# Kernel tuning notes

Measured on AMD Instinct MI355X. Metric: run time of the kernel, lower is better.

The kernel has to match this reference:

```python
import jax, jax.numpy as jnp
import numpy as np

B, C, H, W = 16, 256, 128, 128
NF = 8
GN_GROUPS = 8
EPS = 1e-5


def setup_inputs() -> dict:
    key = jax.random.key(0)
    k0, k1, k2, k3 = jax.random.split(key, 4)
    return {
        "x": jax.random.normal(k0, (B, C, H, W), dtype=jnp.float32),
        # learned params
        "filter_bank": jax.random.normal(k1, (NF, 1, 7, 7), dtype=jnp.float32) * 0.02,
        "sel_w": jax.random.normal(k2, (NF, C), dtype=jnp.float32) / np.float32(np.sqrt(C)),
        "sel_b": jnp.zeros((NF,), dtype=jnp.float32),
        "proj_w": jax.random.normal(k3, (C, C, 1, 1), dtype=jnp.float32) / np.float32(np.sqrt(C)),
        "proj_b": jnp.zeros((C,), dtype=jnp.float32),
        "gn_gamma": jnp.ones((C,), dtype=jnp.float32),
        "gn_beta": jnp.zeros((C,), dtype=jnp.float32),
    }


def reference(x, filter_bank, sel_w, sel_b, proj_w, proj_b, gn_gamma, gn_beta):
    b, c, h, w = x.shape
    # filter selector: GAP -> Linear -> softmax
    pooled = x.mean(axis=(2, 3))                       # [B, C]
    weights = jax.nn.softmax(pooled @ sel_w.T + sel_b, axis=-1)  # [B, NF]
    # softmax-weighted mix of the 7x7 filter bank -> one filter per sample
    combined = jnp.einsum('bn,nhw->bhw', weights, filter_bank[:, 0])  # [B, 7, 7]
    # per-sample depthwise conv: each sample's filter applied to all C channels
    kern = jnp.repeat(combined[:, None], c, axis=0)    # [B*C, 1, 7, 7] (sample-major, matches reshape)
    filtered = jax.lax.conv_general_dilated(
        x.reshape(1, b * c, h, w), kern,
        window_strides=(1, 1), padding=((3, 3), (3, 3)),
        feature_group_count=b * c,
        dimension_numbers=('NCHW', 'OIHW', 'NCHW'),
    ).reshape(b, c, h, w)
    # output projection: 1x1 conv
    y = jnp.einsum('bchw,oc->bohw', filtered, proj_w[:, :, 0, 0]) + proj_b[None, :, None, None]
    # GroupNorm(8, C) with affine
    yg = y.reshape(b, GN_GROUPS, c // GN_GROUPS, h, w)
    mean = yg.mean(axis=(2, 3, 4), keepdims=True)
    var = yg.var(axis=(2, 3, 4), keepdims=True)
    yn = ((yg - mean) * jax.lax.rsqrt(var + EPS)).reshape(b, c, h, w)
    yn = yn * gn_gamma[None, :, None, None] + gn_beta[None, :, None, None]
    # exact GELU (torch default) + residual
    return jax.nn.gelu(yn, approximate=False) + x
```

## Files before the change

kernel.cpp:

```cpp
#include <hip/hip_runtime.h>
#include <math.h>

#define BB 16
#define CC 256
#define HH 128
#define WW 128
#define HWSZ 16384
#define NF 8
#define EPSV 1e-5f

typedef __attribute__((ext_vector_type(8))) short short8;
typedef __attribute__((ext_vector_type(4))) float f32x4;

static __device__ __forceinline__ unsigned short f2bf(float f) {
  unsigned int u = __float_as_uint(f);
  u += 0x7fffu + ((u >> 16) & 1u);
  return (unsigned short)(u >> 16);
}

static __device__ __forceinline__ float bf2f(unsigned int h) {
  return __uint_as_float(h << 16);
}

static __device__ __forceinline__ void gload_lds16(const unsigned short* g,
                                                   unsigned short* l) {
  __builtin_amdgcn_global_load_lds(
      (const __attribute__((address_space(1))) void*)(size_t)g,
      (__attribute__((address_space(3))) void*)(unsigned)(size_t)l, 16, 0, 0);
}

__global__ __launch_bounds__(256) void pack_a_kernel(
    const float* __restrict__ pw, unsigned short* __restrict__ ap) {
  int idx = blockIdx.x * 256 + threadIdx.x;
  int e = idx & 7;
  int lane = (idx >> 3) & 63;
  int kb = (idx >> 9) & 7;
  int mb = idx >> 12;
  int o = mb * 16 + (lane & 15);
  int c = kb * 32 + (lane >> 4) * 8 + e;
  ap[idx] = f2bf(pw[o * 256 + c]);
}

__global__ __launch_bounds__(256) void pool_kernel(
    const float* __restrict__ x, float* __restrict__ pooled) {
  int plane = blockIdx.x;
  const float4* xp = (const float4*)(x + (size_t)plane * HWSZ);
  int tid = threadIdx.x;
  float s = 0.f;
#pragma unroll
  for (int i = 0; i < 16; ++i) {
    float4 v = xp[tid + i * 256];
    s += v.x + v.y + v.z + v.w;
  }
#pragma unroll
  for (int off = 32; off > 0; off >>= 1) s += __shfl_down(s, off, 64);
  __shared__ float ls[4];
  if ((tid & 63) == 0) ls[tid >> 6] = s;
  __syncthreads();
  if (tid == 0) pooled[plane] = (ls[0] + ls[1] + ls[2] + ls[3]) * (1.0f / 16384.0f);
}

__global__ __launch_bounds__(256) void selector_kernel(
    const float* __restrict__ pooled, const float* __restrict__ sel_w,
    const float* __restrict__ sel_b, const float* __restrict__ fbank,
    float* __restrict__ combined) {
  int tid = threadIdx.x;
  __shared__ float lg[BB][NF];
  __shared__ float wsm[BB][NF];
  if (tid < BB * NF) {
    int b = tid >> 3, n = tid & 7;
    const float* p = pooled + b * CC;
    const float* w = sel_w + n * CC;
    float d = sel_b[n];
    for (int c = 0; c < CC; c += 4) {
      d += p[c] * w[c] + p[c + 1] * w[c + 1] + p[c + 2] * w[c + 2] + p[c + 3] * w[c + 3];
    }
    lg[b][n] = d;
  }
  __syncthreads();
  if (tid < BB) {
    int b = tid;
    float m = lg[b][0];
#pragma unroll
    for (int n = 1; n < NF; ++n) m = fmaxf(m, lg[b][n]);
    float e[NF];
    float s = 0.f;
#pragma unroll
    for (int n = 0; n < NF; ++n) { e[n] = expf(lg[b][n] - m); s += e[n]; }
    float inv = 1.0f / s;
#pragma unroll
    for (int n = 0; n < NF; ++n) wsm[b][n] = e[n] * inv;
  }
  __syncthreads();
  for (int i = tid; i < BB * 49; i += 256) {
    int b = i / 49, j = i % 49;
    float acc = 0.f;
#pragma unroll
    for (int n = 0; n < NF; ++n) acc += wsm[b][n] * fbank[n * 49 + j];
    combined[b * 64 + j] = acc;
  }
}

#define TR 32
__global__ __launch_bounds__(256) void dwconv_kernel(
    const float* __restrict__ x, const float* __restrict__ combined,
    unsigned short* __restrict__ fbp) {
  int plane = blockIdx.x;
  int rt = blockIdx.y;
  int b = plane >> 8;
  int r0 = rt * TR;
  int tid = threadIdx.x;

  __shared__ float xs[TR + 6][136];

  float kf[49];
  {
    const float* cb = combined + b * 64;
#pragma unroll
    for (int i = 0; i < 49; ++i) kf[i] = cb[i];
  }

  const size_t pbase = (size_t)plane * HWSZ;
  for (int idx = tid; idx < (TR + 6) * 34; idx += 256) {
    int row = idx / 34;
    int seg = idx % 34;
    int r = r0 - 3 + row;
    int c = seg * 4 - 4;
    float4 v = make_float4(0.f, 0.f, 0.f, 0.f);
    if (r >= 0 && r < HH && c >= 0 && c < WW) {
      v = *(const float4*)(x + pbase + (size_t)r * WW + c);
    }
    *(float4*)&xs[row][seg * 4] = v;
  }
  __syncthreads();

  int cg = tid & 31;
  int rg = tid >> 5;
  float acc[4][4] = {};

#pragma unroll
  for (int ri = 0; ri < 10; ++ri) {
    int lrow = 4 * rg + ri;
    float xr[12];
#pragma unroll
    for (int s = 0; s < 3; ++s)
      *(float4*)&xr[4 * s] = *(const float4*)&xs[lrow][cg * 4 + 4 * s];
#pragma unroll
    for (int orr = 0; orr < 4; ++orr) {
      int dy = ri - orr;
      if (dy < 0 || dy > 6) continue;
#pragma unroll
      for (int oc = 0; oc < 4; ++oc) {
#pragma unroll
        for (int dx = 0; dx < 7; ++dx) {
          acc[orr][oc] += xr[oc + dx + 1] * kf[dy * 7 + dx];
        }
      }
    }
  }

#pragma unroll
  for (int orr = 0; orr < 4; ++orr) {
    ushort4 sv;
    sv.x = f2bf(acc[orr][0]);
    sv.y = f2bf(acc[orr][1]);
    sv.z = f2bf(acc[orr][2]);
    sv.w = f2bf(acc[orr][3]);
    *(ushort4*)(fbp + pbase + (size_t)(r0 + 4 * rg + orr) * WW + 4 * cg) = sv;
  }
}

__global__ __launch_bounds__(256) void transpose_kernel(
    const unsigned short* __restrict__ fb, unsigned short* __restrict__ fbT) {
  int bid = blockIdx.x;
  int bs = bid >> 10;
  int cs = (bid >> 8) & 3;
  int ps = bid & 255;
  int t = threadIdx.x;

  __shared__ unsigned int Ts[64][33];

  int cpair = t >> 3;
  int pch = t & 7;
  const unsigned short* s =
      fb + ((size_t)bs * CC + cs * 64 + 2 * cpair) * HWSZ + ps * 64 + pch * 8;
  uint4 A0 = *(const uint4*)s;
  uint4 A1 = *(const uint4*)(s + HWSZ);
  unsigned int wa[4] = {A0.x, A0.y, A0.z, A0.w};
  unsigned int wb[4] = {A1.x, A1.y, A1.z, A1.w};
#pragma unroll
  for (int i = 0; i < 8; ++i) {
    int p = pch * 8 + i;
    unsigned int lo = (wa[i >> 1] >> ((i & 1) * 16)) & 0xffffu;
    unsigned int hi = (wb[i >> 1] >> ((i & 1) * 16)) & 0xffffu;
    Ts[p][cpair] = lo | (hi << 16);
  }
  __syncthreads();

  size_t obase = ((size_t)bs * HWSZ + (size_t)ps * 64) * 256 + cs * 64;
#pragma unroll
  for (int r = 0; r < 2; ++r) {
    int chunk = t + 256 * r;
    int p = chunk >> 3, ch = chunk & 7;
    uint4 v;
    v.x = Ts[p][ch * 4];
    v.y = Ts[p][ch * 4 + 1];
    v.z = Ts[p][ch * 4 + 2];
    v.w = Ts[p][ch * 4 + 3];
    *(uint4*)(fbT + obase + (size_t)p * 256 + ch * 8) = v;
  }
}

#define SWZ(p) ((((p) >> 1) ^ ((p) >> 4)) & 3)

__global__ __launch_bounds__(512, 4) void gemm_kernel(
    const unsigned short* __restrict__ fbT, const unsigned short* __restrict__ ap,
    const float* __restrict__ proj_b, unsigned short* __restrict__ yb,
    float* __restrict__ part) {
  int bid = blockIdx.x;
  int bs = bid >> 8;
  int ot = (bid >> 7) & 1;
  int pt = bid & 127;
  int p0 = pt * 128;
  int tid = threadIdx.x;
  int lane = tid & 63;
  int wave = tid >> 6;
  int wm = wave >> 2;
  int wn = wave & 3;

  __shared__ __align__(16) unsigned short A_lds[2][4096];
  __shared__ __align__(16) unsigned short B_lds[2][4096];

  const unsigned short* asrc0 =
      ap + (((size_t)(ot * 8 + (tid >> 6)) * 8) * 64 + (tid & 63)) * 8;
  unsigned short* adst = &A_lds[0][0] + (size_t)tid * 8;
  int sp = tid >> 2;
  int sj = (tid & 3) ^ SWZ(sp);
  const unsigned short* bsrc0 =
      fbT + ((size_t)bs * HWSZ + p0 + sp) * 256 + sj * 8;
  unsigned short* bdst = &B_lds[0][0] + (size_t)tid * 8;

#define STAGE(kb, buf)                                                  \
  do {                                                                  \
    gload_lds16(asrc0 + (size_t)(kb) * 512, adst + (size_t)(buf) * 4096); \
    gload_lds16(bsrc0 + (size_t)(kb) * 32, bdst + (size_t)(buf) * 4096);  \
  } while (0)

  STAGE(0, 0);
  STAGE(1, 1);

  f32x4 acc[4][2];
#pragma unroll
  for (int mb = 0; mb < 4; ++mb)
#pragma unroll
    for (int nb = 0; nb < 2; ++nb) acc[mb][nb] = (f32x4){0.f, 0.f, 0.f, 0.f};

  int aofs[4];
#pragma unroll
  for (int mb = 0; mb < 4; ++mb) aofs[mb] = ((wm * 4 + mb) * 64 + lane) * 8;
  int bofs[2];
#pragma unroll
  for (int nb = 0; nb < 2; ++nb) {
    int pp = wn * 32 + nb * 16 + (lane & 15);
    bofs[nb] = pp * 32 + (((lane >> 4) * 8) ^ (SWZ(pp) << 3));
  }

#pragma unroll
  for (int kb = 0; kb < 8; ++kb) {
    const int cur = kb & 1;
    if (kb < 7) {
      asm volatile("s_waitcnt vmcnt(2)" ::: "memory");
    } else {
      asm volatile("s_waitcnt vmcnt(0)" ::: "memory");
    }
    __builtin_amdgcn_s_barrier();

    short8 af[4], bfr[2];
#pragma unroll
    for (int mb = 0; mb < 4; ++mb)
      af[mb] = *(const short8*)(&A_lds[cur][0] + aofs[mb]);
#pragma unroll
    for (int nb = 0; nb < 2; ++nb)
      bfr[nb] = *(const short8*)(&B_lds[cur][0] + bofs[nb]);
    asm volatile("s_waitcnt lgkmcnt(0)" ::: "memory");
    __builtin_amdgcn_sched_barrier(0);
    __builtin_amdgcn_s_barrier();

    if (kb < 6) STAGE(kb + 2, cur);
    __builtin_amdgcn_sched_barrier(0);

#pragma unroll
    for (int mb = 0; mb < 4; ++mb)
#pragma unroll
      for (int nb = 0; nb < 2; ++nb)
        acc[mb][nb] = __builtin_amdgcn_mfma_f32_16x16x32_bf16(
            af[mb], bfr[nb], acc[mb][nb], 0, 0, 0);
  }

  float psum[2] = {0.f, 0.f}, psq[2] = {0.f, 0.f};
  int orl = (lane >> 4) * 4;
  int pl = lane & 15;
  const size_t ybase = (size_t)bs * CC * HWSZ + p0 + wn * 32;
  int obase = ot * 128 + wm * 64;
#pragma unroll
  for (int mb = 0; mb < 4; ++mb) {
    int gi = mb >> 1;
#pragma unroll
    for (int r = 0; r < 4; ++r) {
      int o = obase + mb * 16 + orl + r;
      float pb = proj_b[o];
      unsigned short* yrow = yb + ybase + (size_t)o * HWSZ + pl;
#pragma unroll
      for (int nb = 0; nb < 2; ++nb) {
        float v = acc[mb][nb][r] + pb;
        yrow[nb * 16] = f2bf(v);
        psum[gi] += v;
        psq[gi] += v * v;
      }
    }
  }
#pragma unroll
  for (int off = 32; off > 0; off >>= 1) {
#pragma unroll
    for (int k = 0; k < 2; ++k) {
      psum[k] += __shfl_down(psum[k], off, 64);
      psq[k] += __shfl_down(psq[k], off, 64);
    }
  }
  if (lane == 0) {
#pragma unroll
    for (int k = 0; k < 2; ++k) {
      int bg = bs * 8 + ot * 4 + wm * 2 + k;
      part[(size_t)bg * 512 + pt * 4 + wn] = psum[k];
      part[65536 + (size_t)bg * 512 + pt * 4 + wn] = psq[k];
    }
  }
#undef STAGE
}

__global__ __launch_bounds__(256) void reduce_kernel(
    const float* __restrict__ part, float* __restrict__ stats) {
  int bg = blockIdx.x;
  int t = threadIdx.x;
  const float* ps = part + (size_t)bg * 512;
  const float* pq = part + 65536 + (size_t)bg * 512;
  float s = ps[t] + ps[t + 256];
  float q = pq[t] + pq[t + 256];
#pragma unroll
  for (int off = 32; off > 0; off >>= 1) {
    s += __shfl_down(s, off, 64);
    q += __shfl_down(q, off, 64);
  }
  __shared__ float ls[8];
  if ((t & 63) == 0) { ls[t >> 6] = s; ls[4 + (t >> 6)] = q; }
  __syncthreads();
  if (t == 0) stats[bg] = ls[0] + ls[1] + ls[2] + ls[3];
  if (t == 64) stats[128 + bg] = ls[4] + ls[5] + ls[6] + ls[7];
}

__global__ __launch_bounds__(256) void out_kernel(
    const float* __restrict__ x, const unsigned short* __restrict__ yb,
    const float* __restrict__ stats, const float* __restrict__ gamma,
    const float* __restrict__ beta, float* __restrict__ out) {
  int plane = blockIdx.x;
  int b = plane >> 8, c = plane & 255, g = c >> 5;
  const float inv_n = 1.0f / (32.0f * (float)HWSZ);
  float mean = stats[b * 8 + g] * inv_n;
  float var = stats[128 + b * 8 + g] * inv_n - mean * mean;
  float rstd = rsqrtf(var + EPSV);
  float scale = gamma[c] * rstd;
  float shift = beta[c] - mean * scale;

  const size_t base = (size_t)plane * HWSZ;
  for (int i = threadIdx.x; i < HWSZ / 8; i += 256) {
    uint4 yv = *(const uint4*)(yb + base + 8 * (size_t)i);
    float4 x0 = *(const float4*)(x + base + 8 * (size_t)i);
    float4 x1 = *(const float4*)(x + base + 8 * (size_t)i + 4);
    unsigned int yw[4] = {yv.x, yv.y, yv.z, yv.w};
    float r[8];
    float xr[8] = {x0.x, x0.y, x0.z, x0.w, x1.x, x1.y, x1.z, x1.w};
#pragma unroll
    for (int k = 0; k < 8; ++k) {
      unsigned int h = (yw[k >> 1] >> ((k & 1) * 16)) & 0xffffu;
      float t = bf2f(h) * scale + shift;
      float ge = 0.5f * t * (1.0f + erff(t * 0.70710678118654752f));
      r[k] = ge + xr[k];
    }
    *(float4*)(out + base + 8 * (size_t)i) = make_float4(r[0], r[1], r[2], r[3]);
    *(float4*)(out + base + 8 * (size_t)i + 4) = make_float4(r[4], r[5], r[6], r[7]);
  }
}

extern "C" void kernel_launch(void* const* d_in, const int* in_sizes, int n_in,
                              void* d_out, int out_size, void* d_ws, size_t ws_size,
                              hipStream_t stream) {
  const float* x      = (const float*)d_in[0];
  const float* fbank  = (const float*)d_in[1];
  const float* sel_w  = (const float*)d_in[2];
  const float* sel_b  = (const float*)d_in[3];
  const float* proj_w = (const float*)d_in[4];
  const float* proj_b = (const float*)d_in[5];
  const float* gamma  = (const float*)d_in[6];
  const float* beta   = (const float*)d_in[7];
  float* out = (float*)d_out;

  unsigned short* fb  = (unsigned short*)d_ws;
  unsigned short* yb  = fb;
  unsigned short* fbT = fb + (size_t)BB * CC * HWSZ;
  unsigned short* apk = fbT + (size_t)BB * CC * HWSZ;
  float* pooled   = (float*)(apk + 65536);
  float* combined = pooled + BB * CC;
  float* stats    = combined + BB * 64;
  float* part     = stats + 256;

  hipLaunchKernelGGL(pack_a_kernel, dim3(256), dim3(256), 0, stream, proj_w, apk);
  hipLaunchKernelGGL(pool_kernel, dim3(BB * CC), dim3(256), 0, stream, x, pooled);
  hipLaunchKernelGGL(selector_kernel, dim3(1), dim3(256), 0, stream,
                     pooled, sel_w, sel_b, fbank, combined);
  hipLaunchKernelGGL(dwconv_kernel, dim3(BB * CC, HH / TR), dim3(256), 0, stream,
                     x, combined, fb);
  hipLaunchKernelGGL(transpose_kernel, dim3(BB * 4 * 256), dim3(256), 0, stream,
                     fb, fbT);
  hipLaunchKernelGGL(gemm_kernel, dim3(BB * 2 * 128), dim3(512), 0, stream,
                     fbT, apk, proj_b, yb, part);
  hipLaunchKernelGGL(reduce_kernel, dim3(128), dim3(256), 0, stream, part, stats);
  hipLaunchKernelGGL(out_kernel, dim3(BB * CC), dim3(256), 0, stream,
                     x, yb, stats, gamma, beta, out);
}
```

Before: 456.4 us.

## Widen GEMM tile to all 256 output channels and fuse pool with weight pack

```diff
diff --git a/kernel.cpp b/kernel.cpp
--- a/kernel.cpp
+++ b/kernel.cpp
@@ -29,23 +29,23 @@
       (__attribute__((address_space(3))) void*)(unsigned)(size_t)l, 16, 0, 0);
 }
 
-__global__ __launch_bounds__(256) void pack_a_kernel(
-    const float* __restrict__ pw, unsigned short* __restrict__ ap) {
-  int idx = blockIdx.x * 256 + threadIdx.x;
-  int e = idx & 7;
-  int lane = (idx >> 3) & 63;
-  int kb = (idx >> 9) & 7;
-  int mb = idx >> 12;
-  int o = mb * 16 + (lane & 15);
-  int c = kb * 32 + (lane >> 4) * 8 + e;
-  ap[idx] = f2bf(pw[o * 256 + c]);
-}
-
-__global__ __launch_bounds__(256) void pool_kernel(
-    const float* __restrict__ x, float* __restrict__ pooled) {
-  int plane = blockIdx.x;
-  const float4* xp = (const float4*)(x + (size_t)plane * HWSZ);
+__global__ __launch_bounds__(256) void pool_pack_kernel(
+    const float* __restrict__ x, const float* __restrict__ pw,
+    float* __restrict__ pooled, unsigned short* __restrict__ ap) {
+  int blk = blockIdx.x;
   int tid = threadIdx.x;
+  if (blk >= BB * CC) {
+    int idx = (blk - BB * CC) * 256 + tid;
+    int e = idx & 7;
+    int lane = (idx >> 3) & 63;
+    int kb = (idx >> 9) & 7;
+    int mb = idx >> 12;
+    int o = mb * 16 + (lane & 15);
+    int c = kb * 32 + (lane >> 4) * 8 + e;
+    ap[idx] = f2bf(pw[o * 256 + c]);
+    return;
+  }
+  const float4* xp = (const float4*)(x + (size_t)blk * HWSZ);
   float s = 0.f;
 #pragma unroll
   for (int i = 0; i < 16; ++i) {
@@ -57,7 +57,7 @@
   __shared__ float ls[4];
   if ((tid & 63) == 0) ls[tid >> 6] = s;
   __syncthreads();
-  if (tid == 0) pooled[plane] = (ls[0] + ls[1] + ls[2] + ls[3]) * (1.0f / 16384.0f);
+  if (tid == 0) pooled[blk] = (ls[0] + ls[1] + ls[2] + ls[3]) * (1.0f / 16384.0f);
 }
 
 __global__ __launch_bounds__(256) void selector_kernel(
@@ -213,26 +213,25 @@
 
 #define SWZ(p) ((((p) >> 1) ^ ((p) >> 4)) & 3)
 
-__global__ __launch_bounds__(512, 4) void gemm_kernel(
+__global__ __launch_bounds__(512, 2) void gemm_kernel(
     const unsigned short* __restrict__ fbT, const unsigned short* __restrict__ ap,
     const float* __restrict__ proj_b, unsigned short* __restrict__ yb,
     float* __restrict__ part) {
   int bid = blockIdx.x;
-  int bs = bid >> 8;
-  int ot = (bid >> 7) & 1;
+  int bs = bid >> 7;
   int pt = bid & 127;
   int p0 = pt * 128;
   int tid = threadIdx.x;
   int lane = tid & 63;
   int wave = tid >> 6;
-  int wm = wave >> 2;
-  int wn = wave & 3;
-
-  __shared__ __align__(16) unsigned short A_lds[2][4096];
+  int wm = wave >> 1;
+  int wn = wave & 1;
+
+  __shared__ __align__(16) unsigned short A_lds[2][8192];
   __shared__ __align__(16) unsigned short B_lds[2][4096];
 
   const unsigned short* asrc0 =
-      ap + (((size_t)(ot * 8 + (tid >> 6)) * 8) * 64 + (tid & 63)) * 8;
+      ap + (size_t)(tid >> 6) * 4096 + (size_t)(tid & 63) * 8;
   unsigned short* adst = &A_lds[0][0] + (size_t)tid * 8;
   int sp = tid >> 2;
   int sj = (tid & 3) ^ SWZ(sp);
@@ -240,28 +239,30 @@
       fbT + ((size_t)bs * HWSZ + p0 + sp) * 256 + sj * 8;
   unsigned short* bdst = &B_lds[0][0] + (size_t)tid * 8;
 
-#define STAGE(kb, buf)                                                  \
-  do {                                                                  \
-    gload_lds16(asrc0 + (size_t)(kb) * 512, adst + (size_t)(buf) * 4096); \
-    gload_lds16(bsrc0 + (size_t)(kb) * 32, bdst + (size_t)(buf) * 4096);  \
+#define STAGE(kb, buf)                                                        \
+  do {                                                                        \
+    gload_lds16(asrc0 + (size_t)(kb) * 512, adst + (size_t)(buf) * 8192);     \
+    gload_lds16(asrc0 + 32768 + (size_t)(kb) * 512,                           \
+                adst + (size_t)(buf) * 8192 + 4096);                          \
+    gload_lds16(bsrc0 + (size_t)(kb) * 32, bdst + (size_t)(buf) * 4096);      \
   } while (0)
 
   STAGE(0, 0);
   STAGE(1, 1);
 
-  f32x4 acc[4][2];
+  f32x4 acc[4][4];
 #pragma unroll
   for (int mb = 0; mb < 4; ++mb)
 #pragma unroll
-    for (int nb = 0; nb < 2; ++nb) acc[mb][nb] = (f32x4){0.f, 0.f, 0.f, 0.f};
+    for (int nb = 0; nb < 4; ++nb) acc[mb][nb] = (f32x4){0.f, 0.f, 0.f, 0.f};
 
   int aofs[4];
 #pragma unroll
   for (int mb = 0; mb < 4; ++mb) aofs[mb] = ((wm * 4 + mb) * 64 + lane) * 8;
-  int bofs[2];
-#pragma unroll
-  for (int nb = 0; nb < 2; ++nb) {
-    int pp = wn * 32 + nb * 16 + (lane & 15);
+  int bofs[4];
+#pragma unroll
+  for (int nb = 0; nb < 4; ++nb) {
+    int pp = wn * 64 + nb * 16 + (lane & 15);
     bofs[nb] = pp * 32 + (((lane >> 4) * 8) ^ (SWZ(pp) << 3));
   }
 
@@ -269,18 +270,18 @@
   for (int kb = 0; kb < 8; ++kb) {
     const int cur = kb & 1;
     if (kb < 7) {
-      asm volatile("s_waitcnt vmcnt(2)" ::: "memory");
+      asm volatile("s_waitcnt vmcnt(3)" ::: "memory");
     } else {
       asm volatile("s_waitcnt vmcnt(0)" ::: "memory");
     }
     __builtin_amdgcn_s_barrier();
 
-    short8 af[4], bfr[2];
+    short8 af[4], bfr[4];
 #pragma unroll
     for (int mb = 0; mb < 4; ++mb)
       af[mb] = *(const short8*)(&A_lds[cur][0] + aofs[mb]);
 #pragma unroll
-    for (int nb = 0; nb < 2; ++nb)
+    for (int nb = 0; nb < 4; ++nb)
       bfr[nb] = *(const short8*)(&B_lds[cur][0] + bofs[nb]);
     asm volatile("s_waitcnt lgkmcnt(0)" ::: "memory");
     __builtin_amdgcn_sched_barrier(0);
@@ -292,7 +293,7 @@
 #pragma unroll
     for (int mb = 0; mb < 4; ++mb)
 #pragma unroll
-      for (int nb = 0; nb < 2; ++nb)
+      for (int nb = 0; nb < 4; ++nb)
         acc[mb][nb] = __builtin_amdgcn_mfma_f32_16x16x32_bf16(
             af[mb], bfr[nb], acc[mb][nb], 0, 0, 0);
   }
@@ -300,8 +301,8 @@
   float psum[2] = {0.f, 0.f}, psq[2] = {0.f, 0.f};
   int orl = (lane >> 4) * 4;
   int pl = lane & 15;
-  const size_t ybase = (size_t)bs * CC * HWSZ + p0 + wn * 32;
-  int obase = ot * 128 + wm * 64;
+  const size_t ybase = (size_t)bs * CC * HWSZ + p0 + wn * 64;
+  int obase = wm * 64;
 #pragma unroll
   for (int mb = 0; mb < 4; ++mb) {
     int gi = mb >> 1;
@@ -311,7 +312,7 @@
       float pb = proj_b[o];
       unsigned short* yrow = yb + ybase + (size_t)o * HWSZ + pl;
 #pragma unroll
-      for (int nb = 0; nb < 2; ++nb) {
+      for (int nb = 0; nb < 4; ++nb) {
         float v = acc[mb][nb][r] + pb;
         yrow[nb * 16] = f2bf(v);
         psum[gi] += v;
@@ -330,9 +331,9 @@
   if (lane == 0) {
 #pragma unroll
     for (int k = 0; k < 2; ++k) {
-      int bg = bs * 8 + ot * 4 + wm * 2 + k;
-      part[(size_t)bg * 512 + pt * 4 + wn] = psum[k];
-      part[65536 + (size_t)bg * 512 + pt * 4 + wn] = psq[k];
+      int bg = bs * 8 + wm * 2 + k;
+      part[(size_t)bg * 256 + pt * 2 + wn] = psum[k];
+      part[32768 + (size_t)bg * 256 + pt * 2 + wn] = psq[k];
     }
   }
 #undef STAGE
@@ -342,10 +343,8 @@
     const float* __restrict__ part, float* __restrict__ stats) {
   int bg = blockIdx.x;
   int t = threadIdx.x;
-  const float* ps = part + (size_t)bg * 512;
-  const float* pq = part + 65536 + (size_t)bg * 512;
-  float s = ps[t] + ps[t + 256];
-  float q = pq[t] + pq[t + 256];
+  float s = part[(size_t)bg * 256 + t];
+  float q = part[32768 + (size_t)bg * 256 + t];
 #pragma unroll
   for (int off = 32; off > 0; off >>= 1) {
     s += __shfl_down(s, off, 64);
@@ -413,15 +412,15 @@
   float* stats    = combined + BB * 64;
   float* part     = stats + 256;
 
-  hipLaunchKernelGGL(pack_a_kernel, dim3(256), dim3(256), 0, stream, proj_w, apk);
-  hipLaunchKernelGGL(pool_kernel, dim3(BB * CC), dim3(256), 0, stream, x, pooled);
+  hipLaunchKernelGGL(pool_pack_kernel, dim3(BB * CC + 256), dim3(256), 0, stream,
+                     x, proj_w, pooled, apk);
   hipLaunchKernelGGL(selector_kernel, dim3(1), dim3(256), 0, stream,
                      pooled, sel_w, sel_b, fbank, combined);
   hipLaunchKernelGGL(dwconv_kernel, dim3(BB * CC, HH / TR), dim3(256), 0, stream,
                      x, combined, fb);
   hipLaunchKernelGGL(transpose_kernel, dim3(BB * 4 * 256), dim3(256), 0, stream,
                      fb, fbT);
-  hipLaunchKernelGGL(gemm_kernel, dim3(BB * 2 * 128), dim3(512), 0, stream,
+  hipLaunchKernelGGL(gemm_kernel, dim3(BB * 128), dim3(512), 0, stream,
                      fbT, apk, proj_b, yb, part);
   hipLaunchKernelGGL(reduce_kernel, dim3(128), dim3(256), 0, stream, part, stats);
   hipLaunchKernelGGL(out_kernel, dim3(BB * CC), dim3(256), 0, stream,
```

Result: no change. 454.6 us (-0.4%).
